# Optimization experiments

Measured on AMD Instinct MI355X. Metric: run time of the kernel, lower is better.

The kernel has to match this reference:

```python
import jax, jax.numpy as jnp
import numpy as np

N_NODES = 50000


def gcn_conv(x, src, dst, W, b, n_nodes):
    # x: [N, Fin]; src/dst: [E'] (self-loops already included)
    # PyG GCNConv: h = x @ W; aggregate with norm = deg^{-1/2}[src] * deg^{-1/2}[dst]; + bias
    ones = jnp.ones(src.shape[0], dtype=x.dtype)
    deg = jax.ops.segment_sum(ones, dst, num_segments=n_nodes)  # [N]
    dinv = jnp.where(deg > 0, jax.lax.rsqrt(deg), 0.0)
    norm = dinv[src] * dinv[dst]  # [E']
    h = x @ W  # [N, Fout]
    msgs = h[src] * norm[:, None]  # gather + scale, [E', Fout]
    out = jax.ops.segment_sum(msgs, dst, num_segments=n_nodes)  # scatter-add
    return out + b


def setup_inputs() -> dict:
    key = jax.random.key(0)
    ks = jax.random.split(key, 8)
    n, e = N_NODES, 800000
    in_c, out_c = 64, 32
    hid = 2 * out_c  # 64

    def glorot(k, fan_in, fan_out):
        s = jnp.sqrt(2.0 / (fan_in + fan_out))
        return jax.random.normal(k, (fan_in, fan_out), dtype=jnp.float32) * s

    return {
        "z": jax.random.normal(ks[0], (n, in_c), dtype=jnp.float32),
        "edge_index": jax.random.randint(ks[1], (2, e), 0, n, dtype=jnp.int32),
        "W1": glorot(ks[2], in_c, hid),
        "b1": jnp.zeros((hid,), dtype=jnp.float32),
        "W2": glorot(ks[3], hid, out_c),
        "b2": jnp.zeros((out_c,), dtype=jnp.float32),
        "Wfc": glorot(ks[4], out_c, 1024),
        "bfc": jnp.zeros((1024,), dtype=jnp.float32),
    }


def reference(z, edge_index, W1, b1, W2, b2, Wfc, bfc):
    n = z.shape[0]
    # add self-loops once (same augmented graph used by both convs)
    loops = jnp.arange(n, dtype=edge_index.dtype)
    src = jnp.concatenate([edge_index[0], loops])
    dst = jnp.concatenate([edge_index[1], loops])

    h = jax.nn.relu(gcn_conv(z, src, dst, W1, b1, n))
    h = gcn_conv(h, src, dst, W2, b2, n)
    return h @ Wfc + bfc
```

## Files before the change

kernel.cpp:

```cpp
#include <hip/hip_runtime.h>


#define TB 256
#define FC_ROWS 32
#define SCHUNK 4096
#define FLAGB (1 << 30)

typedef __attribute__((ext_vector_type(2))) float f32x2;


__global__ void k_zero(int4* __restrict__ p, int n4) {
    int i = blockIdx.x * TB + threadIdx.x;
    if (i < n4) p[i] = make_int4(0, 0, 0, 0);
}


__global__ void k_hist(const int* __restrict__ dst, int* __restrict__ cnt,
                       int* __restrict__ slot, int E) {
    int e = blockIdx.x * TB + threadIdx.x;
    if (e < E) slot[e] = atomicAdd(&cnt[dst[e]], 1);
}

__global__ __launch_bounds__(1024)
void k_scanLB(const int* __restrict__ cnt, int* __restrict__ off,
              float* __restrict__ dinv, int* __restrict__ work, int n, int E) {
    __shared__ int wsum[16];
    __shared__ int pfx_s;
    int b = blockIdx.x;
    int i4 = b * SCHUNK + threadIdx.x * 4;
    int lane = threadIdx.x & 63, wid = threadIdx.x >> 6;
    int v0 = 0, v1 = 0, v2 = 0, v3 = 0;
    if (i4 + 3 < n) {
        int4 t = *(const int4*)(cnt + i4);
        v0 = t.x; v1 = t.y; v2 = t.z; v3 = t.w;
    } else {
        if (i4 < n) v0 = cnt[i4];
        if (i4 + 1 < n) v1 = cnt[i4 + 1];
        if (i4 + 2 < n) v2 = cnt[i4 + 2];
        if (i4 + 3 < n) v3 = cnt[i4 + 3];
    }
    if (i4 < n)     dinv[i4]     = rsqrtf((float)(v0 + 1));
    if (i4 + 1 < n) dinv[i4 + 1] = rsqrtf((float)(v1 + 1));
    if (i4 + 2 < n) dinv[i4 + 2] = rsqrtf((float)(v2 + 1));
    if (i4 + 3 < n) dinv[i4 + 3] = rsqrtf((float)(v3 + 1));

    int s = v0 + v1 + v2 + v3;
    int x = s;
#pragma unroll
    for (int ofs = 1; ofs < 64; ofs <<= 1) {
        int t = __shfl_up(x, ofs, 64);
        if (lane >= ofs) x += t;
    }
    if (lane == 63) wsum[wid] = x;
    __syncthreads();
    int wp = 0;
#pragma unroll
    for (int wv = 0; wv < 16; ++wv) wp += (wv < wid) ? wsum[wv] : 0;
    int excl = wp + x - s;

    if (threadIdx.x == 0) {
        int tot = 0;
#pragma unroll
        for (int wv = 0; wv < 16; ++wv) tot += wsum[wv];
        atomicOr(&work[b], tot | FLAGB);
        int pfx = 0;
        for (int j = 0; j < b; ++j) {
            int v;
            do { v = atomicOr(&work[j], 0); } while (!(v & FLAGB));
            pfx += v & (FLAGB - 1);
        }
        pfx_s = pfx;
        if (b == 0) off[n] = E;
    }
    __syncthreads();
    excl += pfx_s;
    if (i4 < n)     off[i4]     = excl;
    if (i4 + 1 < n) off[i4 + 1] = excl + v0;
    if (i4 + 2 < n) off[i4 + 2] = excl + v0 + v1;
    if (i4 + 3 < n) off[i4 + 3] = excl + v0 + v1 + v2;
}

__global__ void k_fill_gemm(const int* __restrict__ src, const int* __restrict__ dst,
                            const int* __restrict__ off, const int* __restrict__ slot,
                            int* __restrict__ eSrc, int E, int fillBlocks,
                            const float* __restrict__ X, const float* __restrict__ W,
                            const float* __restrict__ dinv, float* __restrict__ Y, int n) {
    __shared__ float Ws[64 * 64];
    __shared__ float Xs[16 * 64];
    if ((int)blockIdx.x < fillBlocks) {
        int e = blockIdx.x * TB + threadIdx.x;
        if (e < E) eSrc[off[dst[e]] + slot[e]] = src[e];
        return;
    }
    int gb = blockIdx.x - fillBlocks;
    for (int i = threadIdx.x; i < 64 * 64; i += TB) Ws[i] = W[i];
    int r0 = gb * 16;
    int rows = min(16, n - r0);
    {
        const float4* Xg = (const float4*)(X + (size_t)r0 * 64);
        float4* Xs4 = (float4*)Xs;
        int tot4 = rows * 16;
        for (int i = threadIdx.x; i < tot4; i += TB) Xs4[i] = Xg[i];
    }
    __syncthreads();
    int c = threadIdx.x & 63;
    int g = threadIdx.x >> 6;
#pragma unroll
    for (int rr = 0; rr < 4; ++rr) {
        int rb = g + rr * 4;
        int r = r0 + rb;
        if (r >= n) break;
        const float* x = Xs + rb * 64;
        float acc = 0.f;
#pragma unroll
        for (int k = 0; k < 64; ++k) acc = fmaf(x[k], Ws[k * 64 + c], acc);
        Y[(size_t)r * 64 + c] = acc * dinv[r];
    }
}


__global__ void k_gemm_64_32(const float* __restrict__ X, const float* __restrict__ W,
                             const float* __restrict__ dinv, float* __restrict__ Y, int n) {
    __shared__ float Ws[64 * 32];
    __shared__ float Xs[32 * 64];
    for (int i = threadIdx.x; i < 64 * 32; i += TB) Ws[i] = W[i];
    int r0 = blockIdx.x * 32;
    int rows = min(32, n - r0);
    {
        const float4* Xg = (const float4*)(X + (size_t)r0 * 64);
        float4* Xs4 = (float4*)Xs;
        int tot4 = rows * 16;
        for (int i = threadIdx.x; i < tot4; i += TB) Xs4[i] = Xg[i];
    }
    __syncthreads();
    int c = threadIdx.x & 31;
    int g = threadIdx.x >> 5;
#pragma unroll
    for (int rr = 0; rr < 4; ++rr) {
        int rb = g + rr * 8;
        int r = r0 + rb;
        if (r >= n) break;
        const float* x = Xs + rb * 64;
        float acc = 0.f;
#pragma unroll
        for (int k = 0; k < 64; ++k) acc = fmaf(x[k], Ws[k * 32 + c], acc);
        Y[(size_t)r * 32 + c] = acc * dinv[r];
    }
}


__global__ void k_agg64(const float4* __restrict__ H4, const int* __restrict__ off,
                        const int* __restrict__ eSrc, const float* __restrict__ dinv,
                        const float4* __restrict__ b4, float4* __restrict__ out4, int n) {
    int node = blockIdx.x * 4 + (threadIdx.x >> 6);
    if (node >= n) return;
    int lane = threadIdx.x & 63;
    int feat4 = lane & 7;
    int slot = lane >> 3;
    int j0 = off[node], j1 = off[node + 1];
    float4 lo = make_float4(0.f, 0.f, 0.f, 0.f);
    float4 hi = make_float4(0.f, 0.f, 0.f, 0.f);
    for (int e = j0 + slot; e < j1; e += 8) {
        int s = eSrc[e];
        float4 a = H4[(size_t)s * 16 + feat4];
        float4 b = H4[(size_t)s * 16 + 8 + feat4];
        lo.x += a.x; lo.y += a.y; lo.z += a.z; lo.w += a.w;
        hi.x += b.x; hi.y += b.y; hi.z += b.z; hi.w += b.w;
    }
#pragma unroll
    for (int ofs = 8; ofs < 64; ofs <<= 1) {
        lo.x += __shfl_xor(lo.x, ofs, 64);
        lo.y += __shfl_xor(lo.y, ofs, 64);
        lo.z += __shfl_xor(lo.z, ofs, 64);
        lo.w += __shfl_xor(lo.w, ofs, 64);
        hi.x += __shfl_xor(hi.x, ofs, 64);
        hi.y += __shfl_xor(hi.y, ofs, 64);
        hi.z += __shfl_xor(hi.z, ofs, 64);
        hi.w += __shfl_xor(hi.w, ofs, 64);
    }
    if (slot == 0) {
        float dv = dinv[node];
        float4 s0 = H4[(size_t)node * 16 + feat4];
        float4 s1 = H4[(size_t)node * 16 + 8 + feat4];
        float4 c0 = b4[feat4];
        float4 c1 = b4[feat4 + 8];
        float4 r0, r1;
        r0.x = fmaxf(fmaf(lo.x + s0.x, dv, c0.x), 0.f);
        r0.y = fmaxf(fmaf(lo.y + s0.y, dv, c0.y), 0.f);
        r0.z = fmaxf(fmaf(lo.z + s0.z, dv, c0.z), 0.f);
        r0.w = fmaxf(fmaf(lo.w + s0.w, dv, c0.w), 0.f);
        r1.x = fmaxf(fmaf(hi.x + s1.x, dv, c1.x), 0.f);
        r1.y = fmaxf(fmaf(hi.y + s1.y, dv, c1.y), 0.f);
        r1.z = fmaxf(fmaf(hi.z + s1.z, dv, c1.z), 0.f);
        r1.w = fmaxf(fmaf(hi.w + s1.w, dv, c1.w), 0.f);
        out4[(size_t)node * 16 + feat4] = r0;
        out4[(size_t)node * 16 + 8 + feat4] = r1;
    }
}

__global__ void k_agg32(const float4* __restrict__ H4, const int* __restrict__ off,
                        const int* __restrict__ eSrc, const float* __restrict__ dinv,
                        const float4* __restrict__ b4, float4* __restrict__ out4, int n) {
    int node = blockIdx.x * 4 + (threadIdx.x >> 6);
    if (node >= n) return;
    int lane = threadIdx.x & 63;
    int feat4 = lane & 3;
    int slot = lane >> 2;
    int j0 = off[node], j1 = off[node + 1];
    float4 lo = make_float4(0.f, 0.f, 0.f, 0.f);
    float4 hi = make_float4(0.f, 0.f, 0.f, 0.f);
    for (int e = j0 + slot; e < j1; e += 16) {
        int s = eSrc[e];
        float4 a = H4[(size_t)s * 8 + feat4];
        float4 b = H4[(size_t)s * 8 + 4 + feat4];
        lo.x += a.x; lo.y += a.y; lo.z += a.z; lo.w += a.w;
        hi.x += b.x; hi.y += b.y; hi.z += b.z; hi.w += b.w;
    }
#pragma unroll
    for (int ofs = 4; ofs < 64; ofs <<= 1) {
        lo.x += __shfl_xor(lo.x, ofs, 64);
        lo.y += __shfl_xor(lo.y, ofs, 64);
        lo.z += __shfl_xor(lo.z, ofs, 64);
        lo.w += __shfl_xor(lo.w, ofs, 64);
        hi.x += __shfl_xor(hi.x, ofs, 64);
        hi.y += __shfl_xor(hi.y, ofs, 64);
        hi.z += __shfl_xor(hi.z, ofs, 64);
        hi.w += __shfl_xor(hi.w, ofs, 64);
    }
    if (slot == 0) {
        float dv = dinv[node];
        float4 s0 = H4[(size_t)node * 8 + feat4];
        float4 s1 = H4[(size_t)node * 8 + 4 + feat4];
        float4 c0 = b4[feat4];
        float4 c1 = b4[feat4 + 4];
        float4 r0, r1;
        r0.x = fmaf(lo.x + s0.x, dv, c0.x);
        r0.y = fmaf(lo.y + s0.y, dv, c0.y);
        r0.z = fmaf(lo.z + s0.z, dv, c0.z);
        r0.w = fmaf(lo.w + s0.w, dv, c0.w);
        r1.x = fmaf(hi.x + s1.x, dv, c1.x);
        r1.y = fmaf(hi.y + s1.y, dv, c1.y);
        r1.z = fmaf(hi.z + s1.z, dv, c1.z);
        r1.w = fmaf(hi.w + s1.w, dv, c1.w);
        out4[(size_t)node * 8 + feat4] = r0;
        out4[(size_t)node * 8 + 4 + feat4] = r1;
    }
}

__global__ __launch_bounds__(TB, 4)
void k_fc2(const float* __restrict__ X, const float* __restrict__ W,
           const float* __restrict__ bias, float* __restrict__ Y, int n) {
    __shared__ float Xs[FC_ROWS * 32];
    int c0 = blockIdx.x * 512 + threadIdx.x * 2;
    int r0 = blockIdx.y * FC_ROWS;
    int rows = min(FC_ROWS, n - r0);

    f32x2 w[32];
#pragma unroll
    for (int k = 0; k < 32; ++k) w[k] = *(const f32x2*)(W + k * 1024 + c0);
    f32x2 bb = *(const f32x2*)(bias + c0);

    {
        const float4* Xg = (const float4*)(X + (size_t)r0 * 32);
        float4* Xs4 = (float4*)Xs;
        int tot4 = rows * 8;
        for (int i = threadIdx.x; i < tot4; i += TB) Xs4[i] = Xg[i];
    }
    __syncthreads();

    for (int r = 0; r < rows; ++r) {
        const float* x = Xs + r * 32;
        float a0 = bb.x, a1 = bb.y;
#pragma unroll
        for (int k = 0; k < 32; ++k) {
            float xv = x[k];
            a0 = fmaf(xv, w[k].x, a0);
            a1 = fmaf(xv, w[k].y, a1);
        }
        f32x2 v;
        v.x = a0; v.y = a1;
        __builtin_nontemporal_store(v, (f32x2*)(Y + (size_t)(r0 + r) * 1024 + c0));
    }
}


extern "C" void kernel_launch(void* const* d_in, const int* in_sizes, int n_in,
                              void* d_out, int out_size, void* d_ws, size_t ws_size,
                              hipStream_t stream) {
    const float* z   = (const float*)d_in[0];
    const int*   ei  = (const int*)d_in[1];
    const float* W1  = (const float*)d_in[2];
    const float* b1  = (const float*)d_in[3];
    const float* W2  = (const float*)d_in[4];
    const float* b2  = (const float*)d_in[5];
    const float* Wfc = (const float*)d_in[6];
    const float* bfc = (const float*)d_in[7];
    float* out = (float*)d_out;

    int n = in_sizes[0] / 64;
    int E = in_sizes[1] / 2;
    const int* src = ei;
    const int* dst = ei + E;

    int nPad = (n + 3) & ~3;
    int* cnt    = (int*)d_ws;
    int* work   = cnt + nPad;
    int* off    = work + 16;
    int* slot   = off + (n + 1);
    int* eSrc   = slot + E;
    float* dinv = (float*)(eSrc + E);
    float* bufA = dinv + n;
    float* bufB = bufA + (size_t)n * 64;
    float* h2   = bufA;
    float* agg2 = bufA + (size_t)n * 32;

    int nChunks = (n + SCHUNK - 1) / SCHUNK;

    {
        int n4 = (nPad + 16) / 4;
        k_zero<<<(n4 + TB - 1) / TB, TB, 0, stream>>>((int4*)cnt, n4);
    }
    k_hist<<<(E + TB - 1) / TB, TB, 0, stream>>>(dst, cnt, slot, E);
    k_scanLB<<<nChunks, 1024, 0, stream>>>(cnt, off, dinv, work, n, E);

    {
        int fillBlocks = (E + TB - 1) / TB;
        int gemmBlocks = (n + 15) / 16;
        k_fill_gemm<<<fillBlocks + gemmBlocks, TB, 0, stream>>>(
            src, dst, off, slot, eSrc, E, fillBlocks, z, W1, dinv, bufA, n);
    }

    k_agg64<<<(n + 3) / 4, TB, 0, stream>>>((const float4*)bufA, off, eSrc, dinv,
                                            (const float4*)b1, (float4*)bufB, n);

    k_gemm_64_32<<<(n + 31) / 32, TB, 0, stream>>>(bufB, W2, dinv, h2, n);
    k_agg32<<<(n + 3) / 4, TB, 0, stream>>>((const float4*)h2, off, eSrc, dinv,
                                            (const float4*)b2, (float4*)agg2, n);

    {
        dim3 grid(2, (n + FC_ROWS - 1) / FC_ROWS);
        k_fc2<<<grid, TB, 0, stream>>>(agg2, Wfc, bfc, out, n);
    }
}
```

Measured before the change: 218.2 us.

## Assign one sub-wave group per node in aggregation, drop shuffle reduction

Both aggregation kernels now map a small group of lanes (16 for 64 features, 8 for 32 features) to one node, with each lane owning one float4 of features. Each group walks the node's edge list serially, unrolled by four with separate accumulators to keep several gathers in flight. Previously a full 64-lane wave served each node and split edges across slots, which left many lanes idle at an average degree near 17 and needed a cross-lane shuffle reduction. The new mapping removes the shuffles and packs more nodes per block, at the cost of serial edge loops and load imbalance on high-degree nodes.

```diff
diff --git a/kernel.cpp b/kernel.cpp
--- a/kernel.cpp
+++ b/kernel.cpp
@@ -152,99 +152,77 @@
 __global__ void k_agg64(const float4* __restrict__ H4, const int* __restrict__ off,
                         const int* __restrict__ eSrc, const float* __restrict__ dinv,
                         const float4* __restrict__ b4, float4* __restrict__ out4, int n) {
-    int node = blockIdx.x * 4 + (threadIdx.x >> 6);
+    int node = blockIdx.x * 16 + (threadIdx.x >> 4);
     if (node >= n) return;
-    int lane = threadIdx.x & 63;
-    int feat4 = lane & 7;
-    int slot = lane >> 3;
+    int feat4 = threadIdx.x & 15;
     int j0 = off[node], j1 = off[node + 1];
-    float4 lo = make_float4(0.f, 0.f, 0.f, 0.f);
-    float4 hi = make_float4(0.f, 0.f, 0.f, 0.f);
-    for (int e = j0 + slot; e < j1; e += 8) {
-        int s = eSrc[e];
-        float4 a = H4[(size_t)s * 16 + feat4];
-        float4 b = H4[(size_t)s * 16 + 8 + feat4];
-        lo.x += a.x; lo.y += a.y; lo.z += a.z; lo.w += a.w;
-        hi.x += b.x; hi.y += b.y; hi.z += b.z; hi.w += b.w;
-    }
-#pragma unroll
-    for (int ofs = 8; ofs < 64; ofs <<= 1) {
-        lo.x += __shfl_xor(lo.x, ofs, 64);
-        lo.y += __shfl_xor(lo.y, ofs, 64);
-        lo.z += __shfl_xor(lo.z, ofs, 64);
-        lo.w += __shfl_xor(lo.w, ofs, 64);
-        hi.x += __shfl_xor(hi.x, ofs, 64);
-        hi.y += __shfl_xor(hi.y, ofs, 64);
-        hi.z += __shfl_xor(hi.z, ofs, 64);
-        hi.w += __shfl_xor(hi.w, ofs, 64);
-    }
-    if (slot == 0) {
-        float dv = dinv[node];
-        float4 s0 = H4[(size_t)node * 16 + feat4];
-        float4 s1 = H4[(size_t)node * 16 + 8 + feat4];
-        float4 c0 = b4[feat4];
-        float4 c1 = b4[feat4 + 8];
-        float4 r0, r1;
-        r0.x = fmaxf(fmaf(lo.x + s0.x, dv, c0.x), 0.f);
-        r0.y = fmaxf(fmaf(lo.y + s0.y, dv, c0.y), 0.f);
-        r0.z = fmaxf(fmaf(lo.z + s0.z, dv, c0.z), 0.f);
-        r0.w = fmaxf(fmaf(lo.w + s0.w, dv, c0.w), 0.f);
-        r1.x = fmaxf(fmaf(hi.x + s1.x, dv, c1.x), 0.f);
-        r1.y = fmaxf(fmaf(hi.y + s1.y, dv, c1.y), 0.f);
-        r1.z = fmaxf(fmaf(hi.z + s1.z, dv, c1.z), 0.f);
-        r1.w = fmaxf(fmaf(hi.w + s1.w, dv, c1.w), 0.f);
-        out4[(size_t)node * 16 + feat4] = r0;
-        out4[(size_t)node * 16 + 8 + feat4] = r1;
-    }
+    float4 a0 = make_float4(0.f, 0.f, 0.f, 0.f);
+    float4 a1 = make_float4(0.f, 0.f, 0.f, 0.f);
+    float4 a2 = make_float4(0.f, 0.f, 0.f, 0.f);
+    float4 a3 = make_float4(0.f, 0.f, 0.f, 0.f);
+    int e = j0;
+    for (; e + 4 <= j1; e += 4) {
+        int s0 = eSrc[e], s1 = eSrc[e + 1], s2 = eSrc[e + 2], s3 = eSrc[e + 3];
+        float4 v0 = H4[(size_t)s0 * 16 + feat4];
+        float4 v1 = H4[(size_t)s1 * 16 + feat4];
+        float4 v2 = H4[(size_t)s2 * 16 + feat4];
+        float4 v3 = H4[(size_t)s3 * 16 + feat4];
+        a0.x += v0.x; a0.y += v0.y; a0.z += v0.z; a0.w += v0.w;
+        a1.x += v1.x; a1.y += v1.y; a1.z += v1.z; a1.w += v1.w;
+        a2.x += v2.x; a2.y += v2.y; a2.z += v2.z; a2.w += v2.w;
+        a3.x += v3.x; a3.y += v3.y; a3.z += v3.z; a3.w += v3.w;
+    }
+    for (; e < j1; ++e) {
+        float4 v = H4[(size_t)eSrc[e] * 16 + feat4];
+        a0.x += v.x; a0.y += v.y; a0.z += v.z; a0.w += v.w;
+    }
+    float4 self = H4[(size_t)node * 16 + feat4];
+    float dv = dinv[node];
+    float4 bb = b4[feat4];
+    float4 r;
+    r.x = fmaxf(fmaf((a0.x + a1.x) + (a2.x + a3.x) + self.x, dv, bb.x), 0.f);
+    r.y = fmaxf(fmaf((a0.y + a1.y) + (a2.y + a3.y) + self.y, dv, bb.y), 0.f);
+    r.z = fmaxf(fmaf((a0.z + a1.z) + (a2.z + a3.z) + self.z, dv, bb.z), 0.f);
+    r.w = fmaxf(fmaf((a0.w + a1.w) + (a2.w + a3.w) + self.w, dv, bb.w), 0.f);
+    out4[(size_t)node * 16 + feat4] = r;
 }
 
 __global__ void k_agg32(const float4* __restrict__ H4, const int* __restrict__ off,
                         const int* __restrict__ eSrc, const float* __restrict__ dinv,
                         const float4* __restrict__ b4, float4* __restrict__ out4, int n) {
-    int node = blockIdx.x * 4 + (threadIdx.x >> 6);
+    int node = blockIdx.x * 32 + (threadIdx.x >> 3);
     if (node >= n) return;
-    int lane = threadIdx.x & 63;
-    int feat4 = lane & 3;
-    int slot = lane >> 2;
+    int feat4 = threadIdx.x & 7;
     int j0 = off[node], j1 = off[node + 1];
-    float4 lo = make_float4(0.f, 0.f, 0.f, 0.f);
-    float4 hi = make_float4(0.f, 0.f, 0.f, 0.f);
-    for (int e = j0 + slot; e < j1; e += 16) {
-        int s = eSrc[e];
-        float4 a = H4[(size_t)s * 8 + feat4];
-        float4 b = H4[(size_t)s * 8 + 4 + feat4];
-        lo.x += a.x; lo.y += a.y; lo.z += a.z; lo.w += a.w;
-        hi.x += b.x; hi.y += b.y; hi.z += b.z; hi.w += b.w;
-    }
-#pragma unroll
-    for (int ofs = 4; ofs < 64; ofs <<= 1) {
-        lo.x += __shfl_xor(lo.x, ofs, 64);
-        lo.y += __shfl_xor(lo.y, ofs, 64);
-        lo.z += __shfl_xor(lo.z, ofs, 64);
-        lo.w += __shfl_xor(lo.w, ofs, 64);
-        hi.x += __shfl_xor(hi.x, ofs, 64);
-        hi.y += __shfl_xor(hi.y, ofs, 64);
-        hi.z += __shfl_xor(hi.z, ofs, 64);
-        hi.w += __shfl_xor(hi.w, ofs, 64);
-    }
-    if (slot == 0) {
-        float dv = dinv[node];
-        float4 s0 = H4[(size_t)node * 8 + feat4];
-        float4 s1 = H4[(size_t)node * 8 + 4 + feat4];
-        float4 c0 = b4[feat4];
-        float4 c1 = b4[feat4 + 4];
-        float4 r0, r1;
-        r0.x = fmaf(lo.x + s0.x, dv, c0.x);
-        r0.y = fmaf(lo.y + s0.y, dv, c0.y);
-        r0.z = fmaf(lo.z + s0.z, dv, c0.z);
-        r0.w = fmaf(lo.w + s0.w, dv, c0.w);
-        r1.x = fmaf(hi.x + s1.x, dv, c1.x);
-        r1.y = fmaf(hi.y + s1.y, dv, c1.y);
-        r1.z = fmaf(hi.z + s1.z, dv, c1.z);
-        r1.w = fmaf(hi.w + s1.w, dv, c1.w);
-        out4[(size_t)node * 8 + feat4] = r0;
-        out4[(size_t)node * 8 + 4 + feat4] = r1;
-    }
+    float4 a0 = make_float4(0.f, 0.f, 0.f, 0.f);
+    float4 a1 = make_float4(0.f, 0.f, 0.f, 0.f);
+    float4 a2 = make_float4(0.f, 0.f, 0.f, 0.f);
+    float4 a3 = make_float4(0.f, 0.f, 0.f, 0.f);
+    int e = j0;
+    for (; e + 4 <= j1; e += 4) {
+        int s0 = eSrc[e], s1 = eSrc[e + 1], s2 = eSrc[e + 2], s3 = eSrc[e + 3];
+        float4 v0 = H4[(size_t)s0 * 8 + feat4];
+        float4 v1 = H4[(size_t)s1 * 8 + feat4];
+        float4 v2 = H4[(size_t)s2 * 8 + feat4];
+        float4 v3 = H4[(size_t)s3 * 8 + feat4];
+        a0.x += v0.x; a0.y += v0.y; a0.z += v0.z; a0.w += v0.w;
+        a1.x += v1.x; a1.y += v1.y; a1.z += v1.z; a1.w += v1.w;
+        a2.x += v2.x; a2.y += v2.y; a2.z += v2.z; a2.w += v2.w;
+        a3.x += v3.x; a3.y += v3.y; a3.z += v3.z; a3.w += v3.w;
+    }
+    for (; e < j1; ++e) {
+        float4 v = H4[(size_t)eSrc[e] * 8 + feat4];
+        a0.x += v.x; a0.y += v.y; a0.z += v.z; a0.w += v.w;
+    }
+    float4 self = H4[(size_t)node * 8 + feat4];
+    float dv = dinv[node];
+    float4 bb = b4[feat4];
+    float4 r;
+    r.x = fmaf((a0.x + a1.x) + (a2.x + a3.x) + self.x, dv, bb.x);
+    r.y = fmaf((a0.y + a1.y) + (a2.y + a3.y) + self.y, dv, bb.y);
+    r.z = fmaf((a0.z + a1.z) + (a2.z + a3.z) + self.z, dv, bb.z);
+    r.w = fmaf((a0.w + a1.w) + (a2.w + a3.w) + self.w, dv, bb.w);
+    out4[(size_t)node * 8 + feat4] = r;
 }
 
 __global__ __launch_bounds__(TB, 4)
@@ -330,12 +308,12 @@
             src, dst, off, slot, eSrc, E, fillBlocks, z, W1, dinv, bufA, n);
     }
 
-    k_agg64<<<(n + 3) / 4, TB, 0, stream>>>((const float4*)bufA, off, eSrc, dinv,
-                                            (const float4*)b1, (float4*)bufB, n);
+    k_agg64<<<(n + 15) / 16, TB, 0, stream>>>((const float4*)bufA, off, eSrc, dinv,
+                                              (const float4*)b1, (float4*)bufB, n);
 
     k_gemm_64_32<<<(n + 31) / 32, TB, 0, stream>>>(bufB, W2, dinv, h2, n);
-    k_agg32<<<(n + 3) / 4, TB, 0, stream>>>((const float4*)h2, off, eSrc, dinv,
-                                            (const float4*)b2, (float4*)agg2, n);
+    k_agg32<<<(n + 31) / 32, TB, 0, stream>>>((const float4*)h2, off, eSrc, dinv,
+                                              (const float4*)b2, (float4*)agg2, n);
 
     {
         dim3 grid(2, (n + FC_ROWS - 1) / FC_ROWS);
```

New measurement: 210.9 us. -3.3%, faster.
